# Optimization experiments

Measured on AMD Instinct MI355X. Metric: run time of the kernel, lower is better.

Reference implementation:

```python
import jax, jax.numpy as jnp
import numpy as np

MARGIN = 0.25
SCALE = 64.0
OP = 1.0 + MARGIN
ON = -MARGIN
DELTA_P = 1.0 - MARGIN
DELTA_N = MARGIN
NEG_FILL = -1e4  # effectively -inf for these logits (|logit| < ~300)

B, D = 8192, 1024
N_IDS = 512


def setup_inputs() -> dict:
    key = jax.random.key(0)
    k1, k2 = jax.random.split(key)
    inputs = jax.random.normal(k1, (B, D), dtype=jnp.float32)
    targets = jax.random.randint(k2, (B,), 0, N_IDS, dtype=jnp.int64)
    return {"inputs": inputs, "targets": targets}


def reference(inputs, targets):
    # L2-normalize embeddings (torch F.normalize uses eps=1e-12 clamp on norm)
    norm = jnp.maximum(jnp.linalg.norm(inputs, axis=1, keepdims=True), 1e-12)
    x = inputs / norm
    sim = x @ x.T  # [B, B] cosine similarities

    same = targets[:, None] == targets[None, :]
    eye = jnp.eye(targets.shape[0], dtype=bool)
    pos_mask = same & ~eye
    neg_mask = ~same

    sim_sg = jax.lax.stop_gradient(sim)  # .detach() in original
    ap = jnp.maximum(OP - sim_sg, 0.0)
    an = jnp.maximum(sim_sg - ON, 0.0)

    logit_p = -ap * (sim - DELTA_P) * SCALE
    logit_n = an * (sim - DELTA_N) * SCALE

    lse_p = jax.nn.logsumexp(jnp.where(pos_mask, logit_p, NEG_FILL), axis=1)
    lse_n = jax.nn.logsumexp(jnp.where(neg_mask, logit_n, NEG_FILL), axis=1)

    loss_i = jax.nn.softplus(lse_n + lse_p)  # [B]
    valid = pos_mask.any(axis=1) & neg_mask.any(axis=1)

    total = jnp.sum(jnp.where(valid, loss_i, 0.0))
    count = jnp.maximum(jnp.sum(valid), 1)
    return total / count
```

## Files before the change

### kernel.cpp

```cpp
#include <hip/hip_runtime.h>
#include <hip/hip_bf16.h>
#include <math.h>

#define THREADS 256
typedef unsigned short ushortT;
typedef __attribute__((ext_vector_type(8))) short bf16x8;
typedef __attribute__((ext_vector_type(4))) float f32x4;

__device__ __forceinline__ void async16(const ushortT* g, ushortT* l) {
  __builtin_amdgcn_global_load_lds(
      (const __attribute__((address_space(1))) unsigned int*)g,
      (__attribute__((address_space(3))) unsigned int*)l, 16, 0, 0);
}

__global__ __launch_bounds__(THREADS) void k_rownorm(const float* __restrict__ x,
                                                     float* __restrict__ rnorm,
                                                     int B, int D) {
  const int wave = threadIdx.x >> 6;
  const int lane = threadIdx.x & 63;
  const int row = blockIdx.x * 4 + wave;
  if (row >= B) return;
  const float4* xr = reinterpret_cast<const float4*>(x + (size_t)row * D);
  const int nv = D >> 2;
  float s = 0.f;
  for (int t = lane; t < nv; t += 64) {
    float4 v = xr[t];
    s += v.x * v.x + v.y * v.y + v.z * v.z + v.w * v.w;
  }
  #pragma unroll
  for (int off = 32; off; off >>= 1) s += __shfl_xor(s, off);
  if (lane == 0) rnorm[row] = 1.0f / fmaxf(sqrtf(s), 1e-12f);
}

__device__ __forceinline__ ushortT f2bf(float f) {
  __hip_bfloat16 h = __float2bfloat16(f);
  return *reinterpret_cast<ushortT*>(&h);
}

__global__ __launch_bounds__(THREADS) void k_prep(const float* __restrict__ x,
                                                  const float* __restrict__ rnorm,
                                                  ushortT* __restrict__ xn,
                                                  int B, int D) {
  const int row = blockIdx.x;
  const float rn = rnorm[row];
  const int gid = row * (D / 4) + threadIdx.x;
  float4 v = reinterpret_cast<const float4*>(x)[gid];
  ushort4 o;
  o.x = f2bf(v.x * rn); o.y = f2bf(v.y * rn);
  o.z = f2bf(v.z * rn); o.w = f2bf(v.w * rn);
  reinterpret_cast<ushort4*>(xn)[gid] = o;
}

__global__ __launch_bounds__(THREADS, 2) void k_main_mfma(const ushortT* __restrict__ xn,
                                                          const int* __restrict__ tgt,
                                                          float4* __restrict__ partial,
                                                          int B, int D) {
  __shared__ ushortT Asm[128 * 32];
  __shared__ ushortT Bsm[128 * 32];

  const int tid = threadIdx.x;
  const int lane = tid & 63;
  const int w = tid >> 6;
  const int i0 = blockIdx.x * 128;
  const int j0 = blockIdx.y * 128;
  const int wr = (w >> 1) * 64;
  const int wc = (w & 1) * 64;

  const int sr = lane >> 2;
  const int sc = (lane & 3) ^ (sr & 3);
  const ushortT* gA0 = xn + (size_t)(i0 + w * 16 + sr) * D + sc * 8;
  const ushortT* gA1 = xn + (size_t)(i0 + (w + 4) * 16 + sr) * D + sc * 8;
  const ushortT* gB0 = xn + (size_t)(j0 + w * 16 + sr) * D + sc * 8;
  const ushortT* gB1 = xn + (size_t)(j0 + (w + 4) * 16 + sr) * D + sc * 8;
  ushortT* lA0 = &Asm[w * 512];
  ushortT* lA1 = &Asm[(w + 4) * 512];
  ushortT* lB0 = &Bsm[w * 512];
  ushortT* lB1 = &Bsm[(w + 4) * 512];

  const int fr = lane & 15;
  const int fk = (lane >> 4) ^ (fr & 3);
  const int aoff = (wr + fr) * 32 + fk * 8;
  const int boff = (wc + fr) * 32 + fk * 8;

  f32x4 acc[4][4];
  #pragma unroll
  for (int mt = 0; mt < 4; ++mt)
    #pragma unroll
    for (int nt = 0; nt < 4; ++nt)
      acc[mt][nt] = (f32x4){0.f, 0.f, 0.f, 0.f};

  const int kiters = D / 32;
  for (int kk = 0; kk < kiters; ++kk) {
    const size_t ko = (size_t)kk * 32;
    async16(gA0 + ko, lA0);
    async16(gA1 + ko, lA1);
    async16(gB0 + ko, lB0);
    async16(gB1 + ko, lB1);
    __syncthreads();
    bf16x8 afr[4], bfr[4];
    #pragma unroll
    for (int mt = 0; mt < 4; ++mt)
      afr[mt] = *reinterpret_cast<const bf16x8*>(&Asm[aoff + mt * 512]);
    #pragma unroll
    for (int nt = 0; nt < 4; ++nt)
      bfr[nt] = *reinterpret_cast<const bf16x8*>(&Bsm[boff + nt * 512]);
    #pragma unroll
    for (int mt = 0; mt < 4; ++mt)
      #pragma unroll
      for (int nt = 0; nt < 4; ++nt)
        acc[mt][nt] = __builtin_amdgcn_mfma_f32_16x16x32_bf16(afr[mt], bfr[nt], acc[mt][nt], 0, 0, 0);
    __syncthreads();
  }

  const int cbase = j0 + wc + (lane & 15);
  int tj[4];
  #pragma unroll
  for (int nt = 0; nt < 4; ++nt) tj[nt] = tgt[cbase + nt * 16];

  #pragma unroll
  for (int mt = 0; mt < 4; ++mt) {
    #pragma unroll
    for (int reg = 0; reg < 4; ++reg) {
      const int i = i0 + wr + mt * 16 + (lane >> 4) * 4 + reg;
      const int ti = tgt[i];
      float mp = -1e30f, sp = 0.f, mn = -1e30f, sn = 0.f;
      #pragma unroll
      for (int nt = 0; nt < 4; ++nt) {
        const float sim = acc[mt][nt][reg];
        const int j = cbase + nt * 16;
        const bool same = (tj[nt] == ti);
        {
          const bool v = same && (j != i);
          const float ap = fmaxf(1.25f - sim, 0.f);
          const float lg = -ap * (sim - 0.75f) * 64.f;
          const float nm = v ? fmaxf(mp, lg) : mp;
          sp = sp * __expf(mp - nm) + (v ? __expf(lg - nm) : 0.f);
          mp = nm;
        }
        {
          const bool v = !same;
          const float an = fmaxf(sim + 0.25f, 0.f);
          const float lg = an * (sim - 0.25f) * 64.f;
          const float nm = v ? fmaxf(mn, lg) : mn;
          sn = sn * __expf(mn - nm) + (v ? __expf(lg - nm) : 0.f);
          mn = nm;
        }
      }
      #pragma unroll
      for (int off = 1; off < 16; off <<= 1) {
        float m2 = __shfl_xor(mp, off), s2 = __shfl_xor(sp, off);
        float nm = fmaxf(mp, m2);
        sp = sp * __expf(mp - nm) + s2 * __expf(m2 - nm);
        mp = nm;
        m2 = __shfl_xor(mn, off); s2 = __shfl_xor(sn, off);
        nm = fmaxf(mn, m2);
        sn = sn * __expf(mn - nm) + s2 * __expf(m2 - nm);
        mn = nm;
      }
      if ((lane & 15) == 0) {
        float4 o; o.x = mp; o.y = sp; o.z = mn; o.w = sn;
        partial[((size_t)i * 64 + blockIdx.y) * 2 + (w & 1)] = o;
      }
    }
  }
}

__global__ __launch_bounds__(THREADS) void k_reduce(const float4* __restrict__ partial,
                                                    float* __restrict__ row_loss,
                                                    int B) {
  const int lane = threadIdx.x & 63;
  const int row = blockIdx.x * 4 + (threadIdx.x >> 6);
  const float4 a = partial[(size_t)row * 128 + lane];
  const float4 b = partial[(size_t)row * 128 + 64 + lane];
  float mp = fmaxf(a.x, b.x);
  float sp = a.y * __expf(a.x - mp) + b.y * __expf(b.x - mp);
  float mn = fmaxf(a.z, b.z);
  float sn = a.w * __expf(a.z - mn) + b.w * __expf(b.z - mn);
  #pragma unroll
  for (int off = 1; off < 64; off <<= 1) {
    float m2 = __shfl_xor(mp, off), s2 = __shfl_xor(sp, off);
    float nm = fmaxf(mp, m2);
    sp = sp * __expf(mp - nm) + s2 * __expf(m2 - nm);
    mp = nm;
    m2 = __shfl_xor(mn, off); s2 = __shfl_xor(sn, off);
    nm = fmaxf(mn, m2);
    sn = sn * __expf(mn - nm) + s2 * __expf(m2 - nm);
    mn = nm;
  }
  if (lane == 0) {
    float loss = -1.0f;
    if (sp > 0.f && sn > 0.f) {
      const float z = (mp + logf(sp)) + (mn + logf(sn));
      loss = (z > 0.f) ? (z + log1pf(__expf(-z))) : log1pf(__expf(z));
    }
    row_loss[row] = loss;
  }
}

__global__ __launch_bounds__(THREADS) void k_final(const float* __restrict__ row_loss,
                                                   float* __restrict__ out, int B) {
  __shared__ float ssum[4];
  __shared__ float scnt[4];
  const int tid = threadIdx.x;
  float sum = 0.f, cnt = 0.f;
  for (int i = tid; i < B; i += THREADS) {
    const float l = row_loss[i];
    if (l >= 0.f) { sum += l; cnt += 1.f; }
  }
  #pragma unroll
  for (int off = 32; off; off >>= 1) {
    sum += __shfl_xor(sum, off);
    cnt += __shfl_xor(cnt, off);
  }
  const int wave = tid >> 6;
  const int lane = tid & 63;
  if (lane == 0) { ssum[wave] = sum; scnt[wave] = cnt; }
  __syncthreads();
  if (tid == 0) {
    float ts = 0.f, tc = 0.f;
    #pragma unroll
    for (int w = 0; w < 4; ++w) { ts += ssum[w]; tc += scnt[w]; }
    out[0] = ts / fmaxf(tc, 1.f);
  }
}

extern "C" void kernel_launch(void* const* d_in, const int* in_sizes, int n_in,
                              void* d_out, int out_size, void* d_ws, size_t ws_size,
                              hipStream_t stream) {
  const float* x = (const float*)d_in[0];
  const int* tgt = (const int*)d_in[1];
  float* out = (float*)d_out;
  const int B = in_sizes[1];
  const int D = in_sizes[0] / B;

  float* ws = (float*)d_ws;
  float* rnorm = ws;
  float* row_loss = ws + B;
  ushortT* xn = (ushortT*)(ws + 2 * B);
  float4* partial = (float4*)((char*)d_ws + (size_t)2 * B * 4 + (size_t)B * D * 2);

  k_rownorm<<<B / 4, THREADS, 0, stream>>>(x, rnorm, B, D);
  k_prep<<<B, THREADS, 0, stream>>>(x, rnorm, xn, B, D);
  dim3 g(B / 128, B / 128);
  k_main_mfma<<<g, THREADS, 0, stream>>>(xn, tgt, partial, B, D);
  k_reduce<<<B / 4, THREADS, 0, stream>>>(partial, row_loss, B);
  k_final<<<1, THREADS, 0, stream>>>(row_loss, out, B);
}
```

Baseline: 302.3 us.

## Exploit Gram matrix symmetry with triangular tile grid and simplify negative LSE

The similarity GEMM now launches only upper-triangular 128x128 tiles. Off-diagonal tiles emit row partials for both the i rows and, through a column-wise pass, the j rows, which roughly halves MFMA and load work. Diagonal tiles load a single shared tile. The negative-branch logsumexp drops its running max because the logits are bounded, and the positive branch uses a two-pass max-then-sum instead of online rescaling. Row-norm computation is fused into the bf16 conversion kernel, and the LDS swizzle is replaced by a plain lane-linear layout, which may add bank conflicts. The extra column epilogue adds register pressure.

```diff
diff --git a/kernel.cpp b/kernel.cpp
--- a/kernel.cpp
+++ b/kernel.cpp
@@ -13,38 +13,25 @@
       (__attribute__((address_space(3))) unsigned int*)l, 16, 0, 0);
 }
 
-__global__ __launch_bounds__(THREADS) void k_rownorm(const float* __restrict__ x,
-                                                     float* __restrict__ rnorm,
-                                                     int B, int D) {
-  const int wave = threadIdx.x >> 6;
-  const int lane = threadIdx.x & 63;
-  const int row = blockIdx.x * 4 + wave;
-  if (row >= B) return;
-  const float4* xr = reinterpret_cast<const float4*>(x + (size_t)row * D);
-  const int nv = D >> 2;
-  float s = 0.f;
-  for (int t = lane; t < nv; t += 64) {
-    float4 v = xr[t];
-    s += v.x * v.x + v.y * v.y + v.z * v.z + v.w * v.w;
-  }
-  #pragma unroll
-  for (int off = 32; off; off >>= 1) s += __shfl_xor(s, off);
-  if (lane == 0) rnorm[row] = 1.0f / fmaxf(sqrtf(s), 1e-12f);
-}
-
 __device__ __forceinline__ ushortT f2bf(float f) {
   __hip_bfloat16 h = __float2bfloat16(f);
   return *reinterpret_cast<ushortT*>(&h);
 }
 
 __global__ __launch_bounds__(THREADS) void k_prep(const float* __restrict__ x,
-                                                  const float* __restrict__ rnorm,
-                                                  ushortT* __restrict__ xn,
-                                                  int B, int D) {
+                                                  ushortT* __restrict__ xn, int D) {
+  __shared__ float red[4];
   const int row = blockIdx.x;
-  const float rn = rnorm[row];
-  const int gid = row * (D / 4) + threadIdx.x;
-  float4 v = reinterpret_cast<const float4*>(x)[gid];
+  const int tid = threadIdx.x;
+  const int gid = row * (D / 4) + tid;
+  const float4 v = reinterpret_cast<const float4*>(x)[gid];
+  float s = v.x * v.x + v.y * v.y + v.z * v.z + v.w * v.w;
+  #pragma unroll
+  for (int off = 32; off; off >>= 1) s += __shfl_xor(s, off);
+  if ((tid & 63) == 0) red[tid >> 6] = s;
+  __syncthreads();
+  const float tot = red[0] + red[1] + red[2] + red[3];
+  const float rn = 1.0f / fmaxf(sqrtf(tot), 1e-12f);
   ushort4 o;
   o.x = f2bf(v.x * rn); o.y = f2bf(v.y * rn);
   o.z = f2bf(v.z * rn); o.w = f2bf(v.w * rn);
@@ -54,33 +41,38 @@
 __global__ __launch_bounds__(THREADS, 2) void k_main_mfma(const ushortT* __restrict__ xn,
                                                           const int* __restrict__ tgt,
                                                           float4* __restrict__ partial,
-                                                          int B, int D) {
+                                                          int D, int nb) {
   __shared__ ushortT Asm[128 * 32];
   __shared__ ushortT Bsm[128 * 32];
 
   const int tid = threadIdx.x;
   const int lane = tid & 63;
   const int w = tid >> 6;
-  const int i0 = blockIdx.x * 128;
-  const int j0 = blockIdx.y * 128;
-  const int wr = (w >> 1) * 64;
-  const int wc = (w & 1) * 64;
-
-  const int sr = lane >> 2;
-  const int sc = (lane & 3) ^ (sr & 3);
+
+  const int b = blockIdx.x;
+  int bi = (int)((2.f * nb + 1.f -
+                  sqrtf((2.f * nb + 1.f) * (2.f * nb + 1.f) - 8.f * (float)b)) * 0.5f);
+  while ((bi + 1) * (2 * nb - bi) / 2 <= b) ++bi;
+  while (bi * (2 * nb - bi + 1) / 2 > b) --bi;
+  const int bj = bi + (b - bi * (2 * nb - bi + 1) / 2);
+  const bool isdiag = (bi == bj);
+
+  const int i0 = bi * 128, j0 = bj * 128;
+  const int wr = (w >> 1) * 64, wc = (w & 1) * 64;
+
+  const int sr = lane & 15, sc = lane >> 4;
   const ushortT* gA0 = xn + (size_t)(i0 + w * 16 + sr) * D + sc * 8;
-  const ushortT* gA1 = xn + (size_t)(i0 + (w + 4) * 16 + sr) * D + sc * 8;
+  const ushortT* gA1 = gA0 + (size_t)64 * D;
   const ushortT* gB0 = xn + (size_t)(j0 + w * 16 + sr) * D + sc * 8;
-  const ushortT* gB1 = xn + (size_t)(j0 + (w + 4) * 16 + sr) * D + sc * 8;
+  const ushortT* gB1 = gB0 + (size_t)64 * D;
   ushortT* lA0 = &Asm[w * 512];
   ushortT* lA1 = &Asm[(w + 4) * 512];
   ushortT* lB0 = &Bsm[w * 512];
   ushortT* lB1 = &Bsm[(w + 4) * 512];
 
-  const int fr = lane & 15;
-  const int fk = (lane >> 4) ^ (fr & 3);
-  const int aoff = (wr + fr) * 32 + fk * 8;
-  const int boff = (wc + fr) * 32 + fk * 8;
+  const ushortT* Bbase = isdiag ? Asm : Bsm;
+  const int aoff = ((w >> 1) * 4) * 512 + lane * 8;
+  const int boff = ((w & 1) * 4) * 512 + lane * 8;
 
   f32x4 acc[4][4];
   #pragma unroll
@@ -94,8 +86,10 @@
     const size_t ko = (size_t)kk * 32;
     async16(gA0 + ko, lA0);
     async16(gA1 + ko, lA1);
-    async16(gB0 + ko, lB0);
-    async16(gB1 + ko, lB1);
+    if (!isdiag) {
+      async16(gB0 + ko, lB0);
+      async16(gB1 + ko, lB1);
+    }
     __syncthreads();
     bf16x8 afr[4], bfr[4];
     #pragma unroll
@@ -103,7 +97,7 @@
       afr[mt] = *reinterpret_cast<const bf16x8*>(&Asm[aoff + mt * 512]);
     #pragma unroll
     for (int nt = 0; nt < 4; ++nt)
-      bfr[nt] = *reinterpret_cast<const bf16x8*>(&Bsm[boff + nt * 512]);
+      bfr[nt] = *reinterpret_cast<const bf16x8*>(&Bbase[boff + nt * 512]);
     #pragma unroll
     for (int mt = 0; mt < 4; ++mt)
       #pragma unroll
@@ -112,85 +106,115 @@
     __syncthreads();
   }
 
-  const int cbase = j0 + wc + (lane & 15);
+  const int q = lane >> 4, c = lane & 15;
   int tj[4];
   #pragma unroll
-  for (int nt = 0; nt < 4; ++nt) tj[nt] = tgt[cbase + nt * 16];
-
+  for (int nt = 0; nt < 4; ++nt) tj[nt] = tgt[j0 + wc + nt * 16 + c];
+  int tir[16];
   #pragma unroll
   for (int mt = 0; mt < 4; ++mt) {
+    const int4 t4 = *reinterpret_cast<const int4*>(tgt + i0 + wr + mt * 16 + q * 4);
+    tir[mt * 4 + 0] = t4.x; tir[mt * 4 + 1] = t4.y;
+    tir[mt * 4 + 2] = t4.z; tir[mt * 4 + 3] = t4.w;
+  }
+
+  #pragma unroll
+  for (int mt = 0; mt < 4; ++mt) {
     #pragma unroll
     for (int reg = 0; reg < 4; ++reg) {
-      const int i = i0 + wr + mt * 16 + (lane >> 4) * 4 + reg;
-      const int ti = tgt[i];
-      float mp = -1e30f, sp = 0.f, mn = -1e30f, sn = 0.f;
+      const int i = i0 + wr + mt * 16 + q * 4 + reg;
+      const int ti = tir[mt * 4 + reg];
+      float m = -1e30f, sn = 0.f;
+      float sel[4];
       #pragma unroll
       for (int nt = 0; nt < 4; ++nt) {
-        const float sim = acc[mt][nt][reg];
-        const int j = cbase + nt * 16;
+        const float s = acc[mt][nt][reg];
+        const int j = j0 + wc + nt * 16 + c;
         const bool same = (tj[nt] == ti);
-        {
-          const bool v = same && (j != i);
-          const float ap = fmaxf(1.25f - sim, 0.f);
-          const float lg = -ap * (sim - 0.75f) * 64.f;
-          const float nm = v ? fmaxf(mp, lg) : mp;
-          sp = sp * __expf(mp - nm) + (v ? __expf(lg - nm) : 0.f);
-          mp = nm;
+        const bool vpos = same && (j != i);
+        const float lp = (fminf(s, 1.25f) - 1.25f) * fmaf(s, 64.f, -48.f);
+        const float sv = vpos ? lp : -2e30f;
+        sel[nt] = sv;
+        m = fmaxf(m, sv);
+        const float ln = (fmaxf(s, -0.25f) + 0.25f) * fmaf(s, 64.f, -16.f);
+        const float en = __expf(ln);
+        sn += same ? 0.f : en;
+      }
+      #pragma unroll
+      for (int off = 1; off < 16; off <<= 1) m = fmaxf(m, __shfl_xor(m, off));
+      float sp = 0.f;
+      #pragma unroll
+      for (int nt = 0; nt < 4; ++nt) sp += __expf(sel[nt] - m);
+      #pragma unroll
+      for (int off = 1; off < 16; off <<= 1) {
+        sp += __shfl_xor(sp, off);
+        sn += __shfl_xor(sn, off);
+      }
+      if (c == 0) {
+        float4 o; o.x = m; o.y = sp; o.z = 0.f; o.w = sn;
+        partial[((size_t)i * nb + bj) * 2 + (w & 1)] = o;
+      }
+    }
+  }
+
+  if (!isdiag) {
+    #pragma unroll
+    for (int nt = 0; nt < 4; ++nt) {
+      const int jt = tj[nt];
+      const int jrow = j0 + wc + nt * 16 + c;
+      float m = -1e30f, sn = 0.f;
+      float sel[16];
+      #pragma unroll
+      for (int mt = 0; mt < 4; ++mt) {
+        #pragma unroll
+        for (int reg = 0; reg < 4; ++reg) {
+          const float s = acc[mt][nt][reg];
+          const bool same = (tir[mt * 4 + reg] == jt);
+          const float lp = (fminf(s, 1.25f) - 1.25f) * fmaf(s, 64.f, -48.f);
+          const float sv = same ? lp : -2e30f;
+          sel[mt * 4 + reg] = sv;
+          m = fmaxf(m, sv);
+          const float ln = (fmaxf(s, -0.25f) + 0.25f) * fmaf(s, 64.f, -16.f);
+          const float en = __expf(ln);
+          sn += same ? 0.f : en;
         }
-        {
-          const bool v = !same;
-          const float an = fmaxf(sim + 0.25f, 0.f);
-          const float lg = an * (sim - 0.25f) * 64.f;
-          const float nm = v ? fmaxf(mn, lg) : mn;
-          sn = sn * __expf(mn - nm) + (v ? __expf(lg - nm) : 0.f);
-          mn = nm;
-        }
-      }
-      #pragma unroll
-      for (int off = 1; off < 16; off <<= 1) {
-        float m2 = __shfl_xor(mp, off), s2 = __shfl_xor(sp, off);
-        float nm = fmaxf(mp, m2);
-        sp = sp * __expf(mp - nm) + s2 * __expf(m2 - nm);
-        mp = nm;
-        m2 = __shfl_xor(mn, off); s2 = __shfl_xor(sn, off);
-        nm = fmaxf(mn, m2);
-        sn = sn * __expf(mn - nm) + s2 * __expf(m2 - nm);
-        mn = nm;
-      }
-      if ((lane & 15) == 0) {
-        float4 o; o.x = mp; o.y = sp; o.z = mn; o.w = sn;
-        partial[((size_t)i * 64 + blockIdx.y) * 2 + (w & 1)] = o;
+      }
+      m = fmaxf(m, __shfl_xor(m, 16));
+      m = fmaxf(m, __shfl_xor(m, 32));
+      float sp = 0.f;
+      #pragma unroll
+      for (int k = 0; k < 16; ++k) sp += __expf(sel[k] - m);
+      sp += __shfl_xor(sp, 16); sp += __shfl_xor(sp, 32);
+      sn += __shfl_xor(sn, 16); sn += __shfl_xor(sn, 32);
+      if (lane < 16) {
+        float4 o; o.x = m; o.y = sp; o.z = 0.f; o.w = sn;
+        partial[((size_t)jrow * nb + bi) * 2 + (w >> 1)] = o;
       }
     }
   }
 }
 
 __global__ __launch_bounds__(THREADS) void k_reduce(const float4* __restrict__ partial,
-                                                    float* __restrict__ row_loss,
-                                                    int B) {
+                                                    float* __restrict__ row_loss) {
   const int lane = threadIdx.x & 63;
   const int row = blockIdx.x * 4 + (threadIdx.x >> 6);
   const float4 a = partial[(size_t)row * 128 + lane];
   const float4 b = partial[(size_t)row * 128 + 64 + lane];
   float mp = fmaxf(a.x, b.x);
   float sp = a.y * __expf(a.x - mp) + b.y * __expf(b.x - mp);
-  float mn = fmaxf(a.z, b.z);
-  float sn = a.w * __expf(a.z - mn) + b.w * __expf(b.z - mn);
+  float sn = a.w + b.w;
   #pragma unroll
   for (int off = 1; off < 64; off <<= 1) {
-    float m2 = __shfl_xor(mp, off), s2 = __shfl_xor(sp, off);
-    float nm = fmaxf(mp, m2);
+    const float m2 = __shfl_xor(mp, off), s2 = __shfl_xor(sp, off);
+    const float nm = fmaxf(mp, m2);
     sp = sp * __expf(mp - nm) + s2 * __expf(m2 - nm);
     mp = nm;
-    m2 = __shfl_xor(mn, off); s2 = __shfl_xor(sn, off);
-    nm = fmaxf(mn, m2);
-    sn = sn * __expf(mn - nm) + s2 * __expf(m2 - nm);
-    mn = nm;
+    sn += __shfl_xor(sn, off);
   }
   if (lane == 0) {
     float loss = -1.0f;
     if (sp > 0.f && sn > 0.f) {
-      const float z = (mp + logf(sp)) + (mn + logf(sn));
+      const float z = mp + logf(sp) + logf(sn);
       loss = (z > 0.f) ? (z + log1pf(__expf(-z))) : log1pf(__expf(z));
     }
     row_loss[row] = loss;
@@ -212,9 +236,7 @@
     sum += __shfl_xor(sum, off);
     cnt += __shfl_xor(cnt, off);
   }
-  const int wave = tid >> 6;
-  const int lane = tid & 63;
-  if (lane == 0) { ssum[wave] = sum; scnt[wave] = cnt; }
+  if ((tid & 63) == 0) { ssum[tid >> 6] = sum; scnt[tid >> 6] = cnt; }
   __syncthreads();
   if (tid == 0) {
     float ts = 0.f, tc = 0.f;
@@ -232,17 +254,14 @@
   float* out = (float*)d_out;
   const int B = in_sizes[1];
   const int D = in_sizes[0] / B;
-
-  float* ws = (float*)d_ws;
-  float* rnorm = ws;
-  float* row_loss = ws + B;
-  ushortT* xn = (ushortT*)(ws + 2 * B);
-  float4* partial = (float4*)((char*)d_ws + (size_t)2 * B * 4 + (size_t)B * D * 2);
-
-  k_rownorm<<<B / 4, THREADS, 0, stream>>>(x, rnorm, B, D);
-  k_prep<<<B, THREADS, 0, stream>>>(x, rnorm, xn, B, D);
-  dim3 g(B / 128, B / 128);
-  k_main_mfma<<<g, THREADS, 0, stream>>>(xn, tgt, partial, B, D);
-  k_reduce<<<B / 4, THREADS, 0, stream>>>(partial, row_loss, B);
+  const int nb = B / 128;
+
+  ushortT* xn = (ushortT*)d_ws;
+  float4* partial = (float4*)((char*)d_ws + (size_t)B * D * 2);
+  float* row_loss = (float*)((char*)d_ws + (size_t)B * D * 2 + (size_t)B * 2 * nb * 16);
+
+  k_prep<<<B, THREADS, 0, stream>>>(x, xn, D);
+  k_main_mfma<<<nb * (nb + 1) / 2, THREADS, 0, stream>>>(xn, tgt, partial, D, nb);
+  k_reduce<<<B / 4, THREADS, 0, stream>>>(partial, row_loss);
   k_final<<<1, THREADS, 0, stream>>>(row_loss, out, B);
 }
```

New measurement: 250.4 us. 17.2% less time.
